# Kernel optimization log

Hardware: AMD Instinct MI355X
Metric: run time of the kernel (lower is better)

The kernel has to match this reference:

```python
import jax, jax.numpy as jnp
import numpy as np

B, CIN, COUT, H, W, KK = 1, 32, 64, 181, 360, 4
NNZ_PER, NNZ_PER1 = 9, 4


def _make_psi(rng, K, H, W, nnz_per):
    # Sparse DISCO basis in COO form for longitude 0 (shift-invariant in lon).
    E = K * H * nnz_per
    seg = np.repeat(np.arange(K * H, dtype=np.int32), nnz_per)  # k*H + ho
    ho = seg % H
    dlat = rng.integers(-1, 2, size=E).astype(np.int32)
    hi = np.clip(ho + dlat, 0, H - 1).astype(np.int32)
    wi = (rng.integers(-1, 2, size=E).astype(np.int32)) % W
    vals = (rng.normal(size=E) * 0.2).astype(np.float32)
    return seg, hi, wi, vals


def setup_inputs() -> dict:
    rng = np.random.default_rng(0)
    key = jax.random.key(0)
    ks = jax.random.split(key, 5)
    x = jax.random.normal(ks[0], (B, CIN, H, W), dtype=jnp.float32)
    # spherical quadrature weights: sin(colatitude) * cell area
    theta = np.linspace(0.0, np.pi, H)
    qw = (np.sin(theta) * (np.pi / (H - 1)) * (2.0 * np.pi / W)).astype(np.float32)
    qw = np.maximum(qw, 1e-8).reshape(H, 1)
    seg, hi, wi, vals = _make_psi(rng, KK, H, W, NNZ_PER)
    seg1, hi1, wi1, vals1 = _make_psi(rng, 1, H, W, NNZ_PER1)
    w_depth = jax.random.normal(ks[1], (CIN, KK), dtype=jnp.float32) / np.sqrt(KK)
    w_point = jax.random.normal(ks[2], (COUT, CIN), dtype=jnp.float32) / np.sqrt(CIN)
    bias = jax.random.normal(ks[3], (COUT,), dtype=jnp.float32) * 0.02
    return {
        "x": x,
        "quad_w": jnp.asarray(qw),
        "vals": jnp.asarray(vals),
        "seg": jnp.asarray(seg),
        "hi": jnp.asarray(hi),
        "wi": jnp.asarray(wi),
        "w_depth": w_depth,
        "vals1": jnp.asarray(vals1),
        "seg1": jnp.asarray(seg1),
        "hi1": jnp.asarray(hi1),
        "wi1": jnp.asarray(wi1),
        "w_point": w_point,
        "bias": bias,
        "K": KK,
    }


def _disco_contract(x, vals, seg, hi, wi, K):
    # x: [B,C,H,W]; COO psi at lon 0; out[b,c,k,ho,wo] =
    #   sum_{e: seg[e]==k*H+ho} vals[e] * x[b,c,hi[e],(wi[e]+wo) mod W]
    Bq, C, Hq, Wq = x.shape
    rows = x[:, :, hi, :]                                        # [B,C,E,W]
    col = (wi[:, None] + jnp.arange(Wq, dtype=wi.dtype)[None, :]) % Wq  # [E,W]
    rolled = jnp.take_along_axis(rows, col[None, None, :, :], axis=3)   # [B,C,E,W]
    weighted = rolled * vals[None, None, :, None]
    out = jax.ops.segment_sum(weighted.transpose(2, 0, 1, 3), seg,
                              num_segments=K * Hq)               # [K*H,B,C,W]
    return out.reshape(K, Hq, Bq, C, Wq).transpose(2, 3, 0, 1, 4)  # [B,C,K,H,W]


def reference(x, quad_w, vals, seg, hi, wi, w_depth, vals1, seg1, hi1, wi1,
              w_point, bias, K):
    # depthwise DISCO conv (groups=C_in, no bias)
    xq = x * quad_w                                   # quadrature weighting
    xd = _disco_contract(xq, vals, seg, hi, wi, K)    # [B,C,K,H,W]
    y = jnp.einsum("ck,bckhw->bchw", w_depth, xd)     # per-channel K mix
    # pointwise DISCO conv (kernel_shape=1) = CLinear
    yq = y * quad_w
    z = _disco_contract(yq, vals1, seg1, hi1, wi1, 1)[:, :, 0]  # [B,C,H,W]
    out = jnp.einsum("oc,bchw->bohw", w_point, z) + bias[None, :, None, None]
    return out
```

## Files before the change

kernel.cpp:

```cpp
#include <hip/hip_runtime.h>


#define H_    181
#define W_    360
#define CIN_  32
#define COUT_ 64
#define K_    4
#define NNZ_  9
#define NNZ1_ 4
#define HW_   (H_*W_)
#define NT_   (NNZ1_*K_*NNZ_)
#define CSTRIDE_ (H_*25)
#define PXT_  64

__global__ __launch_bounds__(256) void sepconv_coefs(
    const float* __restrict__ quad_w,
    const float* __restrict__ vals, const int* __restrict__ hi,
    const int* __restrict__ wi, const float* __restrict__ w_depth,
    const float* __restrict__ vals1, const int* __restrict__ hi1,
    const int* __restrict__ wi1, float* __restrict__ Call)
{
    const int h   = blockIdx.x;
    const int tid = threadIdx.x;

    __shared__ float Tval[NT_];
    __shared__ int   Tbin[NT_];
    __shared__ float S[K_][25];

    if (tid < NT_) {
        const int a   = tid / 36;
        const int rem = tid - a * 36;
        const int k   = rem / 9;
        const int j   = rem - k * 9;
        const int e1  = h * NNZ1_ + a;
        const int m   = hi1[e1];
        const int w1  = wi1[e1];
        const int d1  = (w1 == 1) ? 1 : ((w1 == 0) ? 0 : -1);
        const int e   = (k * H_ + m) * NNZ_ + j;
        const int r   = hi[e];
        const int w0  = wi[e];
        const int d   = (w0 == 1) ? 1 : ((w0 == 0) ? 0 : -1);
        Tval[tid] = vals1[e1] * quad_w[m] * vals[e] * quad_w[r];
        Tbin[tid] = (r - h + 2) * 5 + (d1 + d + 2);
    }
    __syncthreads();

    if (tid < K_ * 25) {
        const int k   = tid / 25;
        const int bin = tid - k * 25;
        float s = 0.f;
        #pragma unroll
        for (int a = 0; a < NNZ1_; ++a)
            #pragma unroll
            for (int j = 0; j < NNZ_; ++j) {
                const int t2 = a * 36 + k * 9 + j;
                if (Tbin[t2] == bin) s += Tval[t2];
            }
        S[k][bin] = s;
    }
    __syncthreads();

    for (int item = tid; item < CIN_ * 25; item += 256) {
        const int c   = item / 25;
        const int bin = item - c * 25;
        float acc = 0.f;
        #pragma unroll
        for (int k = 0; k < K_; ++k) acc += w_depth[c * K_ + k] * S[k][bin];
        Call[c * CSTRIDE_ + h * 25 + bin] = acc;
    }
}

__global__ __launch_bounds__(256) void sepconv_stencil(
    const float* __restrict__ x, const float* __restrict__ Call,
    float* __restrict__ z)
{
    const int bx = blockIdx.x;
    const int h  = (bx & 7) * 23 + (bx >> 3);
    if (h >= H_) return;
    const int cseg = blockIdx.y;
    const int tid  = threadIdx.x;

    __shared__ float C[4][25];
    if (tid < 100) {
        const int c4  = tid / 25;
        const int bin = tid - c4 * 25;
        C[c4][bin] = Call[(cseg * 4 + c4) * CSTRIDE_ + h * 25 + bin];
    }
    __syncthreads();

    int rowoff[5];
    #pragma unroll
    for (int rb = 0; rb < 5; ++rb) {
        int r = h - 2 + rb;
        r = (r < 0) ? 0 : ((r > H_ - 1) ? H_ - 1 : r);
        rowoff[rb] = r * W_;
    }

    for (int item = tid; item < 4 * 90; item += 256) {
        const int c4 = item / 90;
        const int g  = item - c4 * 90;
        const int c  = cseg * 4 + c4;
        const int bw = g * 4;
        const int cA = (bw + W_ - 4) % W_;
        const int cB = bw;
        const int cC = (bw + 4) % W_;
        const float* xc = x + c * HW_;
        const float* Cc = &C[c4][0];

        float a0 = 0.f, a1 = 0.f, a2 = 0.f, a3 = 0.f;
        #pragma unroll
        for (int rb = 0; rb < 5; ++rb) {
            const float* xr = xc + rowoff[rb];
            const float4 vA = *(const float4*)(xr + cA);
            const float4 vB = *(const float4*)(xr + cB);
            const float4 vC = *(const float4*)(xr + cC);
            const float k0 = Cc[rb * 5 + 0], k1 = Cc[rb * 5 + 1],
                        k2 = Cc[rb * 5 + 2], k3 = Cc[rb * 5 + 3],
                        k4 = Cc[rb * 5 + 4];
            a0 += k0 * vA.z + k1 * vA.w + k2 * vB.x + k3 * vB.y + k4 * vB.z;
            a1 += k0 * vA.w + k1 * vB.x + k2 * vB.y + k3 * vB.z + k4 * vB.w;
            a2 += k0 * vB.x + k1 * vB.y + k2 * vB.z + k3 * vB.w + k4 * vC.x;
            a3 += k0 * vB.y + k1 * vB.z + k2 * vB.w + k3 * vC.x + k4 * vC.y;
        }
        float4 r4; r4.x = a0; r4.y = a1; r4.z = a2; r4.w = a3;
        *(float4*)(z + c * HW_ + h * W_ + bw) = r4;
    }
}

__global__ __launch_bounds__(256) void sepconv_pointwise(
    const float* __restrict__ z, const float* __restrict__ w_point,
    const float* __restrict__ bias, float* __restrict__ out)
{
    const int p0  = blockIdx.x * PXT_;
    const int tid = threadIdx.x;

    __shared__ float zs[CIN_][PXT_];
    #pragma unroll
    for (int i = tid; i < CIN_ * PXT_; i += 256) {
        const int c = i >> 6;
        const int j = i & (PXT_ - 1);
        const int p = p0 + j;
        zs[c][j] = (p < HW_) ? z[c * HW_ + p] : 0.f;
    }
    __syncthreads();

    const int j  = tid & (PXT_ - 1);
    const int oh = tid >> 6;
    const int p  = p0 + j;
    if (p >= HW_) return;

    float zr[CIN_];
    #pragma unroll
    for (int c = 0; c < CIN_; ++c) zr[c] = zs[c][j];

    const float* wp = w_point + oh * 16 * CIN_;
    float* op = out + oh * 16 * HW_ + p;
    #pragma unroll 4
    for (int oo = 0; oo < 16; ++oo) {
        float acc = bias[oh * 16 + oo];
        #pragma unroll
        for (int c = 0; c < CIN_; ++c) acc += wp[oo * CIN_ + c] * zr[c];
        op[oo * HW_] = acc;
    }
}

extern "C" void kernel_launch(void* const* d_in, const int* in_sizes, int n_in,
                              void* d_out, int out_size, void* d_ws, size_t ws_size,
                              hipStream_t stream) {
    const float* x       = (const float*)d_in[0];
    const float* quad_w  = (const float*)d_in[1];
    const float* vals    = (const float*)d_in[2];
    const int*   hi      = (const int*)d_in[4];
    const int*   wi      = (const int*)d_in[5];
    const float* w_depth = (const float*)d_in[6];
    const float* vals1   = (const float*)d_in[7];
    const int*   hi1     = (const int*)d_in[9];
    const int*   wi1     = (const int*)d_in[10];
    const float* w_point = (const float*)d_in[11];
    const float* bias    = (const float*)d_in[12];

    float* Call = (float*)d_ws;
    float* z    = (float*)((char*)d_ws + (1 << 20));

    sepconv_coefs<<<H_, 256, 0, stream>>>(
        quad_w, vals, hi, wi, w_depth, vals1, hi1, wi1, Call);
    sepconv_stencil<<<dim3(184, 8), 256, 0, stream>>>(x, Call, z);
    sepconv_pointwise<<<(HW_ + PXT_ - 1) / PXT_, 256, 0, stream>>>(
        z, w_point, bias, (float*)d_out);
}
```

Before: 128.1 us.

## Fuse stencil and pointwise channel mix into one kernel via shared memory

Merges the depthwise stencil kernel and the pointwise 1x1 channel-mix kernel into a single kernel. Each block now handles one latitude row and a 64-pixel longitude segment across all 32 input channels, keeps the stencil outputs in padded shared memory, then applies the 64x32 pointwise weights directly. This removes the global round trip of the intermediate z tensor and one kernel launch. In exchange each block carries more work and shared memory, the grid has fewer blocks, and the last segment is partial.

```diff
diff --git a/kernel.cpp b/kernel.cpp
--- a/kernel.cpp
+++ b/kernel.cpp
@@ -11,7 +11,6 @@
 #define HW_   (H_*W_)
 #define NT_   (NNZ1_*K_*NNZ_)
 #define CSTRIDE_ (H_*25)
-#define PXT_  64
 
 __global__ __launch_bounds__(256) void sepconv_coefs(
     const float* __restrict__ quad_w,
@@ -70,21 +69,26 @@
     }
 }
 
-__global__ __launch_bounds__(256) void sepconv_stencil(
+__global__ __launch_bounds__(256) void sepconv_fused(
     const float* __restrict__ x, const float* __restrict__ Call,
-    float* __restrict__ z)
+    const float* __restrict__ w_point, const float* __restrict__ bias,
+    float* __restrict__ out)
 {
     const int bx = blockIdx.x;
     const int h  = (bx & 7) * 23 + (bx >> 3);
     if (h >= H_) return;
-    const int cseg = blockIdx.y;
-    const int tid  = threadIdx.x;
+    const int seg = blockIdx.y;
+    const int w0  = seg * 64;
+    const int pxn = (seg == 5) ? 40 : 64;
+    const int gn  = pxn >> 2;
+    const int tid = threadIdx.x;
 
-    __shared__ float C[4][25];
-    if (tid < 100) {
-        const int c4  = tid / 25;
-        const int bin = tid - c4 * 25;
-        C[c4][bin] = Call[(cseg * 4 + c4) * CSTRIDE_ + h * 25 + bin];
+    __shared__ float C[CIN_][25];
+    __shared__ float zs[64][33];
+
+    for (int i = tid; i < CIN_ * 25; i += 256) {
+        const int c = i / 25, bin = i - c * 25;
+        C[c][bin] = Call[c * CSTRIDE_ + h * 25 + bin];
     }
     __syncthreads();
 
@@ -96,71 +100,57 @@
         rowoff[rb] = r * W_;
     }
 
-    for (int item = tid; item < 4 * 90; item += 256) {
-        const int c4 = item / 90;
-        const int g  = item - c4 * 90;
-        const int c  = cseg * 4 + c4;
-        const int bw = g * 4;
-        const int cA = (bw + W_ - 4) % W_;
-        const int cB = bw;
-        const int cC = (bw + 4) % W_;
-        const float* xc = x + c * HW_;
-        const float* Cc = &C[c4][0];
+    for (int q = tid; q < CIN_ * 16; q += 256) {
+        const int c = q >> 4;
+        const int g = q & 15;
+        if (g < gn) {
+            const int bw = w0 + g * 4;
+            const int cA = (bw + W_ - 4) % W_;
+            const int cB = bw;
+            const int cC = (bw + 4) % W_;
+            const float* xc = x + c * HW_;
+            const float* Cc = &C[c][0];
 
-        float a0 = 0.f, a1 = 0.f, a2 = 0.f, a3 = 0.f;
-        #pragma unroll
-        for (int rb = 0; rb < 5; ++rb) {
-            const float* xr = xc + rowoff[rb];
-            const float4 vA = *(const float4*)(xr + cA);
-            const float4 vB = *(const float4*)(xr + cB);
-            const float4 vC = *(const float4*)(xr + cC);
-            const float k0 = Cc[rb * 5 + 0], k1 = Cc[rb * 5 + 1],
-                        k2 = Cc[rb * 5 + 2], k3 = Cc[rb * 5 + 3],
-                        k4 = Cc[rb * 5 + 4];
-            a0 += k0 * vA.z + k1 * vA.w + k2 * vB.x + k3 * vB.y + k4 * vB.z;
-            a1 += k0 * vA.w + k1 * vB.x + k2 * vB.y + k3 * vB.z + k4 * vB.w;
-            a2 += k0 * vB.x + k1 * vB.y + k2 * vB.z + k3 * vB.w + k4 * vC.x;
-            a3 += k0 * vB.y + k1 * vB.z + k2 * vB.w + k3 * vC.x + k4 * vC.y;
+            float a0 = 0.f, a1 = 0.f, a2 = 0.f, a3 = 0.f;
+            #pragma unroll
+            for (int rb = 0; rb < 5; ++rb) {
+                const float* xr = xc + rowoff[rb];
+                const float4 vA = *(const float4*)(xr + cA);
+                const float4 vB = *(const float4*)(xr + cB);
+                const float4 vC = *(const float4*)(xr + cC);
+                const float k0 = Cc[rb * 5 + 0], k1 = Cc[rb * 5 + 1],
+                            k2 = Cc[rb * 5 + 2], k3 = Cc[rb * 5 + 3],
+                            k4 = Cc[rb * 5 + 4];
+                a0 += k0 * vA.z + k1 * vA.w + k2 * vB.x + k3 * vB.y + k4 * vB.z;
+                a1 += k0 * vA.w + k1 * vB.x + k2 * vB.y + k3 * vB.z + k4 * vB.w;
+                a2 += k0 * vB.x + k1 * vB.y + k2 * vB.z + k3 * vB.w + k4 * vC.x;
+                a3 += k0 * vB.y + k1 * vB.z + k2 * vB.w + k3 * vC.x + k4 * vC.y;
+            }
+            const int p = g * 4;
+            zs[p + 0][c] = a0;
+            zs[p + 1][c] = a1;
+            zs[p + 2][c] = a2;
+            zs[p + 3][c] = a3;
         }
-        float4 r4; r4.x = a0; r4.y = a1; r4.z = a2; r4.w = a3;
-        *(float4*)(z + c * HW_ + h * W_ + bw) = r4;
-    }
-}
-
-__global__ __launch_bounds__(256) void sepconv_pointwise(
-    const float* __restrict__ z, const float* __restrict__ w_point,
-    const float* __restrict__ bias, float* __restrict__ out)
-{
-    const int p0  = blockIdx.x * PXT_;
-    const int tid = threadIdx.x;
-
-    __shared__ float zs[CIN_][PXT_];
-    #pragma unroll
-    for (int i = tid; i < CIN_ * PXT_; i += 256) {
-        const int c = i >> 6;
-        const int j = i & (PXT_ - 1);
-        const int p = p0 + j;
-        zs[c][j] = (p < HW_) ? z[c * HW_ + p] : 0.f;
     }
     __syncthreads();
 
-    const int j  = tid & (PXT_ - 1);
+    const int j  = tid & 63;
     const int oh = tid >> 6;
-    const int p  = p0 + j;
-    if (p >= HW_) return;
+    if (j < pxn) {
+        float zr[CIN_];
+        #pragma unroll
+        for (int c = 0; c < CIN_; ++c) zr[c] = zs[j][c];
 
-    float zr[CIN_];
-    #pragma unroll
-    for (int c = 0; c < CIN_; ++c) zr[c] = zs[c][j];
-
-    const float* wp = w_point + oh * 16 * CIN_;
-    float* op = out + oh * 16 * HW_ + p;
-    #pragma unroll 4
-    for (int oo = 0; oo < 16; ++oo) {
-        float acc = bias[oh * 16 + oo];
-        #pragma unroll
-        for (int c = 0; c < CIN_; ++c) acc += wp[oo * CIN_ + c] * zr[c];
-        op[oo * HW_] = acc;
+        const float* wp = w_point + oh * 16 * CIN_;
+        float* op = out + oh * 16 * HW_ + h * W_ + w0 + j;
+        #pragma unroll 4
+        for (int oo = 0; oo < 16; ++oo) {
+            float acc = bias[oh * 16 + oo];
+            #pragma unroll
+            for (int c = 0; c < CIN_; ++c) acc += wp[oo * CIN_ + c] * zr[c];
+            op[oo * HW_] = acc;
+        }
     }
 }
 
@@ -180,11 +170,9 @@
     const float* bias    = (const float*)d_in[12];
 
     float* Call = (float*)d_ws;
-    float* z    = (float*)((char*)d_ws + (1 << 20));
 
     sepconv_coefs<<<H_, 256, 0, stream>>>(
         quad_w, vals, hi, wi, w_depth, vals1, hi1, wi1, Call);
-    sepconv_stencil<<<dim3(184, 8), 256, 0, stream>>>(x, Call, z);
-    sepconv_pointwise<<<(HW_ + PXT_ - 1) / PXT_, 256, 0, stream>>>(
-        z, w_point, bias, (float*)d_out);
+    sepconv_fused<<<dim3(184, 6), 256, 0, stream>>>(
+        x, Call, w_point, bias, (float*)d_out);
 }
```

After: 119.5 us. 6.7% less time.
